# Performance work log

Hardware: AMD Instinct MI355X
Metric: run time of the kernel (lower is better)

## Reference

```python
import jax, jax.numpy as jnp
import numpy as np

NUM_HEADS = 32
NUM_KV_HEADS = 8
HEAD_DIM = 128
SCALE = 0.08838834764831845  # 1/sqrt(128)
BATCH = 64
BLOCK_SIZE = 256
BLOCKS_PER_SEQ = 16
NUM_BLOCKS = BATCH * BLOCKS_PER_SEQ
CTX_LEN = BLOCKS_PER_SEQ * BLOCK_SIZE  # 4096


def setup_inputs() -> dict:
    key = jax.random.key(0)
    k1, k2, k3, k4, k5 = jax.random.split(key, 5)
    q = jax.random.normal(k1, (BATCH, NUM_HEADS * HEAD_DIM), dtype=jnp.float32)
    k = jax.random.normal(k2, (BATCH, NUM_KV_HEADS * HEAD_DIM), dtype=jnp.float32)
    v = jax.random.normal(k3, (BATCH, NUM_KV_HEADS * HEAD_DIM), dtype=jnp.float32)
    k_cache = jax.random.normal(k4, (NUM_BLOCKS, BLOCK_SIZE, NUM_KV_HEADS, HEAD_DIM), dtype=jnp.float32)
    v_cache = jax.random.normal(k5, (NUM_BLOCKS, BLOCK_SIZE, NUM_KV_HEADS, HEAD_DIM), dtype=jnp.float32)
    # new token for sequence i goes into the last slot of its last block
    slot_mapping = jnp.arange(BATCH, dtype=jnp.int64) * CTX_LEN + (CTX_LEN - 1)
    block_tables = jnp.arange(NUM_BLOCKS, dtype=jnp.int64).reshape(BATCH, BLOCKS_PER_SEQ)
    context_lens = jnp.full((BATCH,), CTX_LEN, dtype=jnp.int64)
    return {"q": q, "k": k, "v": v, "k_cache": k_cache, "v_cache": v_cache,
            "slot_mapping": slot_mapping, "block_tables": block_tables,
            "context_lens": context_lens}


def reference(q, k, v, k_cache, v_cache, slot_mapping, block_tables, context_lens):
    B = q.shape[0]
    qr = q.reshape(B, NUM_HEADS, HEAD_DIM)          # [B,H,dh]
    kr = k.reshape(B, NUM_KV_HEADS, HEAD_DIM)
    vr = v.reshape(B, NUM_KV_HEADS, HEAD_DIM)
    nb, bs = k_cache.shape[0], k_cache.shape[1]
    # store_kvcache: scatter new K/V into flat slot index = block*block_size + off
    kc = k_cache.reshape(nb * bs, NUM_KV_HEADS, HEAD_DIM).at[slot_mapping].set(kr)
    vc = v_cache.reshape(nb * bs, NUM_KV_HEADS, HEAD_DIM).at[slot_mapping].set(vr)
    kc = kc.reshape(nb, bs, NUM_KV_HEADS, HEAD_DIM)
    vc = vc.reshape(nb, bs, NUM_KV_HEADS, HEAD_DIM)
    # paged gather via block table: [B, nblk, bs, kvh, dh] -> [B, S, kvh, dh]
    S = block_tables.shape[1] * bs
    kg = kc[block_tables].reshape(B, S, NUM_KV_HEADS, HEAD_DIM)
    vg = vc[block_tables].reshape(B, S, NUM_KV_HEADS, HEAD_DIM)
    # GQA expand: repeat_interleave along head dim
    rep = NUM_HEADS // NUM_KV_HEADS
    kg = jnp.repeat(kg, rep, axis=2)                # [B,S,H,dh]
    vg = jnp.repeat(vg, rep, axis=2)
    # single-query causal attention == full attention over context_len keys
    scores = jnp.einsum("bhd,bshd->bhs", qr, kg) * SCALE  # [B,H,S]
    pos = jnp.arange(S)[None, None, :]
    valid = pos < context_lens[:, None, None]
    scores = jnp.where(valid, scores, jnp.float32(-1e30))
    attn = jax.nn.softmax(scores, axis=-1)
    o = jnp.einsum("bhs,bshd->bhd", attn, vg)       # [B,H,dh]
    return o.reshape(B, NUM_HEADS * HEAD_DIM)
```

## Files before the change

kernel.cpp:

```cpp
#include <hip/hip_runtime.h>

#define BATCH 64
#define NH 32
#define NKV 8
#define GQA 4
#define HD 128
#define SEQ 4096
#define BS 256
#define BPS 16
#define QK_SCALE 0.08838834764831845f

__device__ __forceinline__ long long load_idx(const void* p, int i, bool is64) {
    return is64 ? ((const long long*)p)[i] : (long long)((const int*)p)[i];
}

__global__ __launch_bounds__(256, 2) void pa_decode(
    const float* __restrict__ q,
    const float* __restrict__ knew,
    const float* __restrict__ vnew,
    const float* __restrict__ kc,
    const float* __restrict__ vc,
    const void* __restrict__ slot_mapping,
    const void* __restrict__ block_tables,
    const void* __restrict__ context_lens,
    float* __restrict__ out)
{
    const int g    = blockIdx.x;
    const int b    = blockIdx.y;
    const int tid  = threadIdx.x;
    const int wave = tid >> 6;
    const int lane = tid & 63;
    const int grp  = lane >> 3;
    const int l8   = lane & 7;

    const bool is64 = (((const int*)block_tables)[1] == 0);
    const long long ctx    = load_idx(context_lens, b, is64);
    const long long target = load_idx(slot_mapping, b, is64);

    __shared__ int bt_s[BPS];
    __shared__ __align__(16) float acc_lds[4][GQA][HD];
    __shared__ float m_lds[4][GQA];
    __shared__ float l_lds[4][GQA];

    if (tid < BPS) bt_s[tid] = (int)load_idx(block_tables, b * BPS + tid, is64);
    __syncthreads();

    float4 qs[GQA][4];
#pragma unroll
    for (int h = 0; h < GQA; ++h) {
#pragma unroll
        for (int i = 0; i < 4; ++i) {
            float4 t = *(const float4*)(q + (size_t)b * NH * HD + (g * GQA + h) * HD + (i * 8 + l8) * 4);
            qs[h][i] = make_float4(t.x * QK_SCALE, t.y * QK_SCALE, t.z * QK_SCALE, t.w * QK_SCALE);
        }
    }

    float4 acc[GQA][4];
    float m_run[GQA], l_run[GQA];
#pragma unroll
    for (int h = 0; h < GQA; ++h) {
        m_run[h] = -1e30f;
        l_run[h] = 0.f;
#pragma unroll
        for (int i = 0; i < 4; ++i) acc[h][i] = make_float4(0.f, 0.f, 0.f, 0.f);
    }

    const float* knew_b = knew + ((size_t)b * NKV + g) * HD;
    const float* vnew_b = vnew + ((size_t)b * NKV + g) * HD;

    const int s0 = wave * (SEQ / 4);

#pragma unroll 2
    for (int t = 0; t < (SEQ / 4) / 8; ++t) {
        const int s = s0 + t * 8 + grp;
        const int blk = bt_s[s >> 8];
        const long long slot = (long long)blk * BS + (s & (BS - 1));
        const bool isnew = (slot == target);
        const float* kb = isnew ? knew_b : (kc + ((size_t)slot * NKV + g) * HD);
        const float* vb = isnew ? vnew_b : (vc + ((size_t)slot * NKV + g) * HD);

        float4 kv[4], vv[4];
#pragma unroll
        for (int i = 0; i < 4; ++i) kv[i] = *(const float4*)(kb + (i * 8 + l8) * 4);
#pragma unroll
        for (int i = 0; i < 4; ++i) vv[i] = *(const float4*)(vb + (i * 8 + l8) * 4);

        float sc[GQA];
#pragma unroll
        for (int h = 0; h < GQA; ++h) {
            float a = 0.f;
#pragma unroll
            for (int i = 0; i < 4; ++i) {
                a += qs[h][i].x * kv[i].x;
                a += qs[h][i].y * kv[i].y;
                a += qs[h][i].z * kv[i].z;
                a += qs[h][i].w * kv[i].w;
            }
            sc[h] = a;
        }
#pragma unroll
        for (int h = 0; h < GQA; ++h) {
            sc[h] += __shfl_xor(sc[h], 1);
            sc[h] += __shfl_xor(sc[h], 2);
            sc[h] += __shfl_xor(sc[h], 4);
        }

        const bool valid = (s < ctx);
#pragma unroll
        for (int h = 0; h < GQA; ++h) if (!valid) sc[h] = -1e30f;

        float mt[GQA];
#pragma unroll
        for (int h = 0; h < GQA; ++h) {
            float mv = sc[h];
            mv = fmaxf(mv, __shfl_xor(mv, 8));
            mv = fmaxf(mv, __shfl_xor(mv, 16));
            mv = fmaxf(mv, __shfl_xor(mv, 32));
            mt[h] = mv;
        }

#pragma unroll
        for (int h = 0; h < GQA; ++h) {
            if (mt[h] > m_run[h]) {
                const float scl = __expf(m_run[h] - mt[h]);
                m_run[h] = mt[h];
                l_run[h] *= scl;
#pragma unroll
                for (int i = 0; i < 4; ++i) {
                    acc[h][i].x *= scl; acc[h][i].y *= scl;
                    acc[h][i].z *= scl; acc[h][i].w *= scl;
                }
            }
        }

        float p[GQA];
#pragma unroll
        for (int h = 0; h < GQA; ++h) {
            p[h] = valid ? __expf(sc[h] - m_run[h]) : 0.f;
            float ps = p[h];
            ps += __shfl_xor(ps, 8);
            ps += __shfl_xor(ps, 16);
            ps += __shfl_xor(ps, 32);
            l_run[h] += ps;
        }

#pragma unroll
        for (int h = 0; h < GQA; ++h) {
#pragma unroll
            for (int i = 0; i < 4; ++i) {
                acc[h][i].x += p[h] * vv[i].x;
                acc[h][i].y += p[h] * vv[i].y;
                acc[h][i].z += p[h] * vv[i].z;
                acc[h][i].w += p[h] * vv[i].w;
            }
        }
    }

#pragma unroll
    for (int h = 0; h < GQA; ++h) {
#pragma unroll
        for (int i = 0; i < 4; ++i) {
            acc[h][i].x += __shfl_xor(acc[h][i].x, 8);
            acc[h][i].x += __shfl_xor(acc[h][i].x, 16);
            acc[h][i].x += __shfl_xor(acc[h][i].x, 32);
            acc[h][i].y += __shfl_xor(acc[h][i].y, 8);
            acc[h][i].y += __shfl_xor(acc[h][i].y, 16);
            acc[h][i].y += __shfl_xor(acc[h][i].y, 32);
            acc[h][i].z += __shfl_xor(acc[h][i].z, 8);
            acc[h][i].z += __shfl_xor(acc[h][i].z, 16);
            acc[h][i].z += __shfl_xor(acc[h][i].z, 32);
            acc[h][i].w += __shfl_xor(acc[h][i].w, 8);
            acc[h][i].w += __shfl_xor(acc[h][i].w, 16);
            acc[h][i].w += __shfl_xor(acc[h][i].w, 32);
        }
    }

    if (grp == 0) {
#pragma unroll
        for (int h = 0; h < GQA; ++h) {
#pragma unroll
            for (int i = 0; i < 4; ++i)
                *(float4*)&acc_lds[wave][h][(i * 8 + l8) * 4] = acc[h][i];
            if (l8 == 0) { m_lds[wave][h] = m_run[h]; l_lds[wave][h] = l_run[h]; }
        }
    }
    __syncthreads();

    for (int o = tid; o < GQA * HD; o += 256) {
        const int h = o >> 7;
        const int d = o & (HD - 1);
        float mm = -1e30f;
#pragma unroll
        for (int w = 0; w < 4; ++w) mm = fmaxf(mm, m_lds[w][h]);
        float num = 0.f, den = 0.f;
#pragma unroll
        for (int w = 0; w < 4; ++w) {
            const float wt = __expf(m_lds[w][h] - mm);
            num += wt * acc_lds[w][h][d];
            den += wt * l_lds[w][h];
        }
        out[(size_t)b * NH * HD + (g * GQA + h) * HD + d] = num / den;
    }
}

extern "C" void kernel_launch(void* const* d_in, const int* in_sizes, int n_in,
                              void* d_out, int out_size, void* d_ws, size_t ws_size,
                              hipStream_t stream) {
    const float* q    = (const float*)d_in[0];
    const float* k    = (const float*)d_in[1];
    const float* v    = (const float*)d_in[2];
    const float* kc   = (const float*)d_in[3];
    const float* vc   = (const float*)d_in[4];
    const void*  slot = d_in[5];
    const void*  bt   = d_in[6];
    const void*  cl   = d_in[7];
    float* out = (float*)d_out;

    dim3 grid(NKV, BATCH);
    pa_decode<<<grid, 256, 0, stream>>>(q, k, v, kc, vc, slot, bt, cl, out);
}
```

Before: 369.6 us.

## Prefetch next KV tile, defer softmax rescale, bound loop by context length

Restructures the decode loop so the next K/V tile is loaded with nontemporal loads while the current tile is computed, a manual register double buffer. The online-softmax rescale now happens only when some score exceeds the running max by a threshold, which skips the per-iteration cross-group max reduction and the per-iteration sum reduction. The row sum is reduced once at the end instead. The loop trip count is derived from the context length, and masking is applied only to a tail iteration. This costs extra registers for the prefetch buffers, which may lower occupancy, and the deferred rescale relies on exp of up to the threshold staying numerically safe.

```diff
diff --git a/kernel.cpp b/kernel.cpp
--- a/kernel.cpp
+++ b/kernel.cpp
@@ -9,9 +9,17 @@
 #define BS 256
 #define BPS 16
 #define QK_SCALE 0.08838834764831845f
+#define DEFER_THR 8.0f
+
+typedef float f32x4 __attribute__((ext_vector_type(4)));
 
 __device__ __forceinline__ long long load_idx(const void* p, int i, bool is64) {
     return is64 ? ((const long long*)p)[i] : (long long)((const int*)p)[i];
+}
+
+__device__ __forceinline__ float4 ldnt(const float* p) {
+    f32x4 v = __builtin_nontemporal_load(reinterpret_cast<const f32x4*>(p));
+    return make_float4(v.x, v.y, v.z, v.w);
 }
 
 __global__ __launch_bounds__(256, 2) void pa_decode(
@@ -70,60 +78,54 @@
 
     const int s0 = wave * (SEQ / 4);
 
-#pragma unroll 2
-    for (int t = 0; t < (SEQ / 4) / 8; ++t) {
+    const long long cr = ctx - (long long)s0;
+    const int rem = (int)(cr < 0 ? 0 : (cr > 1024 ? 1024 : cr));
+    const int nt  = rem >> 3;
+    const bool tail = (rem & 7) != 0;
+
+    auto mkaddr = [&](int t, const float*& kb, const float*& vb) {
         const int s = s0 + t * 8 + grp;
         const int blk = bt_s[s >> 8];
         const long long slot = (long long)blk * BS + (s & (BS - 1));
         const bool isnew = (slot == target);
-        const float* kb = isnew ? knew_b : (kc + ((size_t)slot * NKV + g) * HD);
-        const float* vb = isnew ? vnew_b : (vc + ((size_t)slot * NKV + g) * HD);
-
-        float4 kv[4], vv[4];
-#pragma unroll
-        for (int i = 0; i < 4; ++i) kv[i] = *(const float4*)(kb + (i * 8 + l8) * 4);
-#pragma unroll
-        for (int i = 0; i < 4; ++i) vv[i] = *(const float4*)(vb + (i * 8 + l8) * 4);
-
+        kb = isnew ? knew_b : (kc + ((size_t)slot * NKV + g) * HD);
+        vb = isnew ? vnew_b : (vc + ((size_t)slot * NKV + g) * HD);
+    };
+
+    auto compute = [&](const float4 (&kvt)[4], const float4 (&vvt)[4], int t, bool masked) {
         float sc[GQA];
 #pragma unroll
         for (int h = 0; h < GQA; ++h) {
             float a = 0.f;
 #pragma unroll
             for (int i = 0; i < 4; ++i) {
-                a += qs[h][i].x * kv[i].x;
-                a += qs[h][i].y * kv[i].y;
-                a += qs[h][i].z * kv[i].z;
-                a += qs[h][i].w * kv[i].w;
-            }
+                a += qs[h][i].x * kvt[i].x;
+                a += qs[h][i].y * kvt[i].y;
+                a += qs[h][i].z * kvt[i].z;
+                a += qs[h][i].w * kvt[i].w;
+            }
+            a += __shfl_xor(a, 1);
+            a += __shfl_xor(a, 2);
+            a += __shfl_xor(a, 4);
             sc[h] = a;
         }
+        if (masked) {
+            const int s = s0 + t * 8 + grp;
+            if ((long long)s >= ctx) {
+#pragma unroll
+                for (int h = 0; h < GQA; ++h) sc[h] = -1e30f;
+            }
+        }
 #pragma unroll
         for (int h = 0; h < GQA; ++h) {
-            sc[h] += __shfl_xor(sc[h], 1);
-            sc[h] += __shfl_xor(sc[h], 2);
-            sc[h] += __shfl_xor(sc[h], 4);
-        }
-
-        const bool valid = (s < ctx);
-#pragma unroll
-        for (int h = 0; h < GQA; ++h) if (!valid) sc[h] = -1e30f;
-
-        float mt[GQA];
-#pragma unroll
-        for (int h = 0; h < GQA; ++h) {
-            float mv = sc[h];
-            mv = fmaxf(mv, __shfl_xor(mv, 8));
-            mv = fmaxf(mv, __shfl_xor(mv, 16));
-            mv = fmaxf(mv, __shfl_xor(mv, 32));
-            mt[h] = mv;
-        }
-
-#pragma unroll
-        for (int h = 0; h < GQA; ++h) {
-            if (mt[h] > m_run[h]) {
-                const float scl = __expf(m_run[h] - mt[h]);
-                m_run[h] = mt[h];
+            if (__any(sc[h] > m_run[h] + DEFER_THR)) {
+                float mv = sc[h];
+                mv = fmaxf(mv, __shfl_xor(mv, 8));
+                mv = fmaxf(mv, __shfl_xor(mv, 16));
+                mv = fmaxf(mv, __shfl_xor(mv, 32));
+                const float newm = fmaxf(m_run[h], mv);
+                const float scl = __expf(m_run[h] - newm);
+                m_run[h] = newm;
                 l_run[h] *= scl;
 #pragma unroll
                 for (int i = 0; i < 4; ++i) {
@@ -131,33 +133,58 @@
                     acc[h][i].z *= scl; acc[h][i].w *= scl;
                 }
             }
-        }
-
-        float p[GQA];
-#pragma unroll
-        for (int h = 0; h < GQA; ++h) {
-            p[h] = valid ? __expf(sc[h] - m_run[h]) : 0.f;
-            float ps = p[h];
-            ps += __shfl_xor(ps, 8);
-            ps += __shfl_xor(ps, 16);
-            ps += __shfl_xor(ps, 32);
-            l_run[h] += ps;
-        }
-
-#pragma unroll
-        for (int h = 0; h < GQA; ++h) {
+            const float p = __expf(sc[h] - m_run[h]);
+            l_run[h] += p;
 #pragma unroll
             for (int i = 0; i < 4; ++i) {
-                acc[h][i].x += p[h] * vv[i].x;
-                acc[h][i].y += p[h] * vv[i].y;
-                acc[h][i].z += p[h] * vv[i].z;
-                acc[h][i].w += p[h] * vv[i].w;
-            }
-        }
+                acc[h][i].x += p * vvt[i].x;
+                acc[h][i].y += p * vvt[i].y;
+                acc[h][i].z += p * vvt[i].z;
+                acc[h][i].w += p * vvt[i].w;
+            }
+        }
+    };
+
+    float4 kv[4], vv[4], kv2[4], vv2[4];
+
+    if (nt > 0) {
+        const float *kb, *vb;
+        mkaddr(0, kb, vb);
+#pragma unroll
+        for (int i = 0; i < 4; ++i) kv[i] = ldnt(kb + (i * 8 + l8) * 4);
+#pragma unroll
+        for (int i = 0; i < 4; ++i) vv[i] = ldnt(vb + (i * 8 + l8) * 4);
+    }
+
+#pragma unroll 2
+    for (int t = 0; t < nt; ++t) {
+        if (t + 1 < nt) {
+            const float *kb, *vb;
+            mkaddr(t + 1, kb, vb);
+#pragma unroll
+            for (int i = 0; i < 4; ++i) kv2[i] = ldnt(kb + (i * 8 + l8) * 4);
+#pragma unroll
+            for (int i = 0; i < 4; ++i) vv2[i] = ldnt(vb + (i * 8 + l8) * 4);
+        }
+        compute(kv, vv, t, false);
+#pragma unroll
+        for (int i = 0; i < 4; ++i) { kv[i] = kv2[i]; vv[i] = vv2[i]; }
+    }
+    if (tail) {
+        const float *kb, *vb;
+        mkaddr(nt, kb, vb);
+#pragma unroll
+        for (int i = 0; i < 4; ++i) kv[i] = ldnt(kb + (i * 8 + l8) * 4);
+#pragma unroll
+        for (int i = 0; i < 4; ++i) vv[i] = ldnt(vb + (i * 8 + l8) * 4);
+        compute(kv, vv, nt, true);
     }
 
 #pragma unroll
     for (int h = 0; h < GQA; ++h) {
+        l_run[h] += __shfl_xor(l_run[h], 8);
+        l_run[h] += __shfl_xor(l_run[h], 16);
+        l_run[h] += __shfl_xor(l_run[h], 32);
 #pragma unroll
         for (int i = 0; i < 4; ++i) {
             acc[h][i].x += __shfl_xor(acc[h][i].x, 8);
```

Result: faster. 313.6 us (-15.2%).
